# Performance work log

Hardware: AMD Instinct MI355X
Metric: run time of the kernel (lower is better)

Reference implementation:

```python
import jax, jax.numpy as jnp
import numpy as np

NU, NI = 50000, 50000
N = NU + NI
NNZ = 1_000_000
DIM = 64          # dim_latent
FK = 4            # factor_k
DK = DIM // FK    # dim_k = 16
ITER_K = 2        # iterate_k
NUM_LAYER = 2     # len(dim_layer_list)
EPS = 1e-12


def setup_inputs() -> dict:
    key = jax.random.key(0)
    k1, k2, k3, k4 = jax.random.split(key, 4)
    # xavier-ish init scale for the embedding tables
    embed_user = jax.random.normal(k1, (NU, DIM), dtype=jnp.float32) * 0.1
    embed_item = jax.random.normal(k2, (NI, DIM), dtype=jnp.float32) * 0.1
    edge_head = jax.random.randint(k3, (NNZ,), 0, N, dtype=jnp.int32)
    edge_tail = jax.random.randint(k4, (NNZ,), 0, N, dtype=jnp.int32)
    return {"embed_user": embed_user, "embed_item": embed_item,
            "edge_head": edge_head, "edge_tail": edge_tail}


def _l2norm(x, axis=-1):
    # torch F.normalize(p=2): x / max(||x||, eps)
    return x / jnp.maximum(jnp.linalg.norm(x, axis=axis, keepdims=True), EPS)


def _dgcf_forward(embed_user, embed_item, head, tail):
    ego = jnp.concatenate([embed_user, embed_item], axis=0)  # [N, DIM]
    A_values = jnp.ones((FK, NNZ), dtype=ego.dtype)
    all_embed = [ego]

    def spmm(v, x):
        # sparse A (values v on edges head->tail) @ x : [N, DK]
        return jax.ops.segment_sum(v[:, None] * x[tail], head, num_segments=N)

    spmm_f = jax.vmap(spmm)  # over factor axis

    for _ in range(NUM_LAYER):
        # split ego into factor chunks: [FK, N, DK]
        xs = jnp.moveaxis(ego.reshape(N, FK, DK), 1, 0)
        factor_emb = None
        for t in range(ITER_K):
            # softmax over factors per edge; detached (as in torch .detach())
            vals = jax.lax.stop_gradient(jax.nn.softmax(A_values, axis=0))  # [FK, NNZ]
            # row sums of each factor adjacency -> D = diag(1/sqrt(rowsum))
            row_sum = jax.ops.segment_sum(vals.T, head, num_segments=N).T   # [FK, N]
            d = jnp.where(row_sum > 0,
                          1.0 / jnp.sqrt(jnp.maximum(row_sum, EPS)), 0.0)
            # factor_emb = D @ A @ D @ x  (three chained spmm in torch)
            y = spmm_f(vals, d[:, :, None] * xs)
            factor_emb = d[:, :, None] * y                                   # [FK, N, DK]
            # routing scores: sum over dim of normalize(h) * tanh(normalize(t))
            h = _l2norm(factor_emb[:, head, :], -1)                          # [FK, NNZ, DK]
            tt = _l2norm(xs[:, tail, :], -1)
            scores = jnp.sum(h * jnp.tanh(tt), axis=-1)                      # [FK, NNZ]
            A_values = A_values + scores
        # layer output: normalize last-iteration factor embeddings, re-concat
        layer_emb = _l2norm(factor_emb, -1)           # [FK, N, DK]
        ego = jnp.moveaxis(layer_emb, 0, 1).reshape(N, DIM)
        all_embed.append(ego)

    out = jnp.mean(jnp.stack(all_embed, axis=1), axis=1)  # [N, DIM]
    return out


def reference(embed_user, embed_item, edge_head, edge_tail):
    out = _dgcf_forward(embed_user, embed_item, edge_head, edge_tail)
    return out[:NU], out[NU:]
```

## Files before the change

### kernel.cpp

```cpp
#include <hip/hip_runtime.h>
#include <hip/hip_bf16.h>

#define NUSER 50000
#define NITEM 50000
#define NN    100000
#define NNZ_  1000000
#define DIM_  64
#define NBLK  391
#define EPB   2560
#define BINC  4096
#define NPAD  (NBLK * BINC)

#define FL_SVC    1
#define FL_SC     2
#define FL_NEXT   8
#define FL_FIN    16
#define FL_ACONST 32
#define FL_ASTORE 64
#define FL_GN     128

static inline int ceil_div(int a, int b) { return (a + b - 1) / b; }

static __device__ inline float bf2f(unsigned short u) {
    return __uint_as_float(((unsigned int)u) << 16);
}
static __device__ inline unsigned short f2bf(float f) {
    unsigned int x = __float_as_uint(f);
    x += 0x7fffu + ((x >> 16) & 1u);
    return (unsigned short)(x >> 16);
}

#if __has_builtin(__builtin_amdgcn_fdot2_f32_bf16)
typedef __bf16 bf16x2_t __attribute__((ext_vector_type(2)));
static __device__ inline float dot2bf(unsigned int a, unsigned int b, float c) {
    return __builtin_amdgcn_fdot2_f32_bf16(__builtin_bit_cast(bf16x2_t, a),
                                           __builtin_bit_cast(bf16x2_t, b), c, false);
}
#else
static __device__ inline float dot2bf(unsigned int a, unsigned int b, float c) {
    return c + bf2f((unsigned short)(a & 0xffffu)) * bf2f((unsigned short)(b & 0xffffu))
             + bf2f((unsigned short)(a >> 16)) * bf2f((unsigned short)(b >> 16));
}
#endif

__global__ void k_binscat(const int* __restrict__ head, const int* __restrict__ tail,
                          int* __restrict__ cursor, int* __restrict__ bin) {
    __shared__ int cnt[NBLK];
    __shared__ int chunk[NBLK];
    int tid = threadIdx.x;
    for (int i = tid; i < NBLK; i += 256) cnt[i] = 0;
    __syncthreads();
    int e0 = blockIdx.x * EPB;
    int e1 = min(e0 + EPB, NNZ_);
    for (int e = e0 + tid; e < e1; e += 256)
        atomicAdd(&cnt[head[e] >> 8], 1);
    __syncthreads();
    for (int i = tid; i < NBLK; i += 256) {
        chunk[i] = cnt[i] ? (i * BINC + atomicAdd(&cursor[i], cnt[i])) : 0;
        cnt[i] = 0;
    }
    __syncthreads();
    for (int e = e0 + tid; e < e1; e += 256) {
        int h = head[e], t = tail[e];
        int b = h >> 8;
        int off = atomicAdd(&cnt[b], 1);
        bin[chunk[b] + off] = t | ((h & 255) << 20);
    }
}

__global__ void k_bucket(const int* __restrict__ bin, const int* __restrict__ cursor,
                         int2* __restrict__ row_se, float4* __restrict__ d4a,
                         int* __restrict__ csr_tail) {
    __shared__ int deg[256];
    __shared__ int sh[256];
    __shared__ int cur[256];
    int tid = threadIdx.x;
    int b = blockIdx.x;
    int n0 = b << 8;
    int e0 = b * BINC, e1 = e0 + cursor[b];
    deg[tid] = 0;
    __syncthreads();
    for (int e = e0 + tid; e < e1; e += 256)
        atomicAdd(&deg[bin[e] >> 20], 1);
    __syncthreads();
    int myDeg = deg[tid];
    sh[tid] = myDeg;
    __syncthreads();
    for (int off = 1; off < 256; off <<= 1) {
        int u = 0;
        if (tid >= off) u = sh[tid - off];
        __syncthreads();
        sh[tid] += u;
        __syncthreads();
    }
    int loff = sh[tid] - myDeg;
    int start = b * BINC + loff;
    int n = n0 + tid;
    if (n < NN) {
        row_se[n] = make_int2(start, start + myDeg);
        float dd = (myDeg > 0) ? 2.0f / sqrtf((float)myDeg) : 0.0f;
        d4a[n] = make_float4(dd, dd, dd, dd);
    }
    cur[tid] = start;
    __syncthreads();
    for (int e = e0 + tid; e < e1; e += 256) {
        int p = bin[e];
        int pos = atomicAdd(&cur[p >> 20], 1);
        csr_tail[pos] = p & 0xFFFFF;
    }
}

__global__ void k_init(const float* __restrict__ eu, const float* __restrict__ ei,
                       const float* __restrict__ d4a,
                       unsigned short* __restrict__ ego, unsigned short* __restrict__ te,
                       unsigned short* __restrict__ G0, float* __restrict__ out) {
    int i = blockIdx.x * 256 + threadIdx.x;
    if (i >= NN * DIM_) return;
    float v = (i < NUSER * DIM_) ? eu[i] : ei[i - NUSER * DIM_];
    out[i] = v;
    ego[i] = f2bf(v);
    G0[i] = f2bf(v * d4a[i >> 4]);
    float s = v * v;
    s += __shfl_xor(s, 1); s += __shfl_xor(s, 2);
    s += __shfl_xor(s, 4); s += __shfl_xor(s, 8);
    float nrm = v / fmaxf(sqrtf(s), 1e-12f);
    float ex = __expf(2.0f * nrm);
    te[i] = f2bf((ex - 1.0f) / (ex + 1.0f));
}

template<int FLAGS, int NJ>
static __device__ __forceinline__ void iter_body(
    int n, int lane, int q, int l, int f, int r0, int r1,
    unsigned short* __restrict__ svals,
    const unsigned short* __restrict__ G,
    const unsigned short* __restrict__ te,
    const int* __restrict__ csr_tail,
    float* __restrict__ A4,
    float* __restrict__ out,
    const unsigned short* __restrict__ X,
    unsigned short* __restrict__ Gn,
    unsigned short* __restrict__ egon, unsigned short* __restrict__ ten)
{
    float ax = 0.f, ay = 0.f, az = 0.f, aw = 0.f;

    int ct[NJ]; float cw[NJ]; float ca[NJ]; uint2 cv[NJ];
    int eb = r0 + q;
#pragma unroll
    for (int j = 0; j < NJ; ++j) {
        int i = eb + 4 * j;
        bool v = (i < r1);
        int ic = v ? i : r0;
        int t = csr_tail[ic];
        ct[j] = v ? t : 0;
        float w;
        if (FLAGS & FL_SVC) w = 1.0f;
        else w = bf2f(svals[ic * 4 + f]);
        cw[j] = v ? w : 0.f;
        if ((FLAGS & FL_SC) && !(FLAGS & FL_ACONST))
            ca[j] = A4[ic * 4 + f];
    }
#pragma unroll
    for (int j = 0; j < NJ; ++j) {
        if (FLAGS & FL_SC)
            cv[j] = *(const uint2*)(te + ct[j] * 64 + 4 * l);
    }
#pragma unroll
    for (int j = 0; j < NJ; ++j) {
        ushort4 u = *(const ushort4*)(G + ct[j] * 64 + 4 * l);
        ax += cw[j] * bf2f(u.x); ay += cw[j] * bf2f(u.y);
        az += cw[j] * bf2f(u.z); aw += cw[j] * bf2f(u.w);
    }

    if (NJ == 4) {
        for (int base = r0 + 16; base < r1; base += 16) {
            int tj[4]; float wj[4];
#pragma unroll
            for (int j = 0; j < 4; ++j) {
                int i = base + q + 4 * j;
                bool v = (i < r1);
                int ic = v ? i : r0;
                int t = csr_tail[ic];
                tj[j] = v ? t : 0;
                float w;
                if (FLAGS & FL_SVC) w = 1.0f;
                else w = bf2f(svals[ic * 4 + f]);
                wj[j] = v ? w : 0.f;
            }
#pragma unroll
            for (int j = 0; j < 4; ++j) {
                ushort4 u = *(const ushort4*)(G + tj[j] * 64 + 4 * l);
                ax += wj[j] * bf2f(u.x); ay += wj[j] * bf2f(u.y);
                az += wj[j] * bf2f(u.z); aw += wj[j] * bf2f(u.w);
            }
        }
    }

    ax += __shfl_xor(ax, 16); ax += __shfl_xor(ax, 32);
    ay += __shfl_xor(ay, 16); ay += __shfl_xor(ay, 32);
    az += __shfl_xor(az, 16); az += __shfl_xor(az, 32);
    aw += __shfl_xor(aw, 16); aw += __shfl_xor(aw, 32);

    float s = ax * ax + ay * ay + az * az + aw * aw;
    s += __shfl_xor(s, 1); s += __shfl_xor(s, 2);
    float inv = 1.0f / fmaxf(sqrtf(s), 1e-12f);
    float fx = ax * inv, fy = ay * inv, fz = az * inv, fw = aw * inv;

    float y = 0.f;
    if (FLAGS & (FL_NEXT | FL_FIN)) {
        int src = lane >> 2;
        float t0r = __shfl(fx, src), t1r = __shfl(fy, src);
        float t2r = __shfl(fz, src), t3r = __shfl(fw, src);
        y = (lane & 2) ? ((lane & 1) ? t3r : t2r) : ((lane & 1) ? t1r : t0r);
        int base = n * 64 + lane;
        if (FLAGS & FL_FIN) {
            out[base] = (out[base] + bf2f(X[base]) + y) * (1.0f / 3.0f);
        }
        if (FLAGS & FL_NEXT) {
            egon[base] = f2bf(y);
            float e2 = __expf(2.0f * y);
            ten[base] = f2bf((e2 - 1.0f) / (e2 + 1.0f));
        }
    }

    float accs = 0.f;
    if (FLAGS & FL_SC) {
        unsigned int p01 = ((unsigned int)f2bf(fy) << 16) | f2bf(fx);
        unsigned int p23 = ((unsigned int)f2bf(fw) << 16) | f2bf(fz);
#pragma unroll
        for (int j = 0; j < NJ; ++j) {
            int i = eb + 4 * j;
            bool v = (i < r1);
            float dot = dot2bf(cv[j].y, p23, dot2bf(cv[j].x, p01, 0.0f));
            dot += __shfl_xor(dot, 1); dot += __shfl_xor(dot, 2);
            float a = (FLAGS & FL_ACONST) ? 1.0f : ca[j];
            a += dot;
            float ex = __expf(a);
            float sum = ex;
            sum += __shfl_xor(sum, 4); sum += __shfl_xor(sum, 8);
            float sv = ex / sum;
            if (v && (l & 3) == 0) {
                if (FLAGS & FL_ASTORE) A4[i * 4 + f] = a;
                svals[i * 4 + f] = f2bf(sv);
            }
            accs += v ? sv : 0.f;
        }
        if (NJ == 4) {
            for (int base = r0 + 16; base < r1; base += 16) {
                int tj[4]; float aj[4]; uint2 vj[4];
#pragma unroll
                for (int j = 0; j < 4; ++j) {
                    int i = base + q + 4 * j;
                    bool v = (i < r1);
                    int ic = v ? i : r0;
                    int t = csr_tail[ic];
                    tj[j] = v ? t : 0;
                    if (!(FLAGS & FL_ACONST)) aj[j] = A4[ic * 4 + f];
                }
#pragma unroll
                for (int j = 0; j < 4; ++j)
                    vj[j] = *(const uint2*)(te + tj[j] * 64 + 4 * l);
#pragma unroll
                for (int j = 0; j < 4; ++j) {
                    int i = base + q + 4 * j;
                    bool v = (i < r1);
                    float dot = dot2bf(vj[j].y, p23, dot2bf(vj[j].x, p01, 0.0f));
                    dot += __shfl_xor(dot, 1); dot += __shfl_xor(dot, 2);
                    float a = (FLAGS & FL_ACONST) ? 1.0f : aj[j];
                    a += dot;
                    float ex = __expf(a);
                    float sum = ex;
                    sum += __shfl_xor(sum, 4); sum += __shfl_xor(sum, 8);
                    float sv = ex / sum;
                    if (v && (l & 3) == 0) {
                        if (FLAGS & FL_ASTORE) A4[i * 4 + f] = a;
                        svals[i * 4 + f] = f2bf(sv);
                    }
                    accs += v ? sv : 0.f;
                }
            }
        }
        accs += __shfl_xor(accs, 16); accs += __shfl_xor(accs, 32);
    }

    if (FLAGS & (FL_GN | FL_NEXT)) {
        float av = __shfl(accs, (lane >> 4) << 2);
        float d = (av > 0.f) ? 1.0f / sqrtf(fmaxf(av, 1e-12f)) : 0.f;
        int base = n * 64 + lane;
        float src = (FLAGS & FL_NEXT) ? y : bf2f(X[base]);
        Gn[base] = f2bf(src * d);
    }
}

template<int FLAGS>
__global__ void k_iter(unsigned short* __restrict__ svals,
                       const unsigned short* __restrict__ G,
                       const unsigned short* __restrict__ te,
                       const int2* __restrict__ row_se, const int* __restrict__ csr_tail,
                       float* __restrict__ A4,
                       float* __restrict__ out,
                       const unsigned short* __restrict__ X,
                       unsigned short* __restrict__ Gn,
                       unsigned short* __restrict__ egon, unsigned short* __restrict__ ten) {
    int n = (blockIdx.x * 256 + threadIdx.x) >> 6;
    if (n >= NN) return;
    int lane = threadIdx.x & 63;
    int q = lane >> 4;
    int l = lane & 15;
    int f = l >> 2;
    int2 se = row_se[n];
    int r0 = __builtin_amdgcn_readfirstlane(se.x);
    int r1 = __builtin_amdgcn_readfirstlane(se.y);
    int deg = r1 - r0;
    if (deg <= 8) {
        if (deg <= 4)
            iter_body<FLAGS, 1>(n, lane, q, l, f, r0, r1, svals, G, te,
                                csr_tail, A4, out, X, Gn, egon, ten);
        else
            iter_body<FLAGS, 2>(n, lane, q, l, f, r0, r1, svals, G, te,
                                csr_tail, A4, out, X, Gn, egon, ten);
    } else {
        if (deg <= 12)
            iter_body<FLAGS, 3>(n, lane, q, l, f, r0, r1, svals, G, te,
                                csr_tail, A4, out, X, Gn, egon, ten);
        else
            iter_body<FLAGS, 4>(n, lane, q, l, f, r0, r1, svals, G, te,
                                csr_tail, A4, out, X, Gn, egon, ten);
    }
}

extern "C" void kernel_launch(void* const* d_in, const int* in_sizes, int n_in,
                              void* d_out, int out_size, void* d_ws, size_t ws_size,
                              hipStream_t stream) {
    const float* eu = (const float*)d_in[0];
    const float* ei = (const float*)d_in[1];
    const int* head = (const int*)d_in[2];
    const int* tail = (const int*)d_in[3];
    float* out = (float*)d_out;

    float* A4 = (float*)d_ws;
    float* d4a = A4 + (size_t)NPAD * 4;
    unsigned short* svals = (unsigned short*)(d4a + (size_t)NN * 4);
    unsigned short* ego_a = svals + (size_t)NPAD * 4;
    unsigned short* te_a  = ego_a + (size_t)NN * DIM_;
    unsigned short* ego_b = te_a + (size_t)NN * DIM_;
    unsigned short* te_b  = ego_b + (size_t)NN * DIM_;
    unsigned short* Ga    = te_b + (size_t)NN * DIM_;
    unsigned short* Gb    = Ga + (size_t)NN * DIM_;
    int* csr_tail = (int*)(Gb + (size_t)NN * DIM_);
    int2* row_se = (int2*)(csr_tail + (size_t)NPAD);
    int* cursor = (int*)(row_se + NN);
    int* bin = (int*)A4;

    const int node_blocks = ceil_div(NN * DIM_, 256);
    const int wave_blocks = ceil_div(NN * 64, 256);

    hipMemsetAsync(cursor, 0, NBLK * sizeof(int), stream);
    k_binscat<<<NBLK, 256, 0, stream>>>(head, tail, cursor, bin);
    k_bucket<<<NBLK, 256, 0, stream>>>(bin, cursor, row_se, (float4*)d4a, csr_tail);

    k_init<<<node_blocks, 256, 0, stream>>>(eu, ei, d4a, ego_a, te_a, Ga, out);

    k_iter<FL_SVC | FL_SC | FL_ACONST | FL_ASTORE | FL_GN><<<wave_blocks, 256, 0, stream>>>(
        svals, Ga, te_a, row_se, csr_tail, A4, out, ego_a, Gb, ego_b, te_b);

    k_iter<FL_SC | FL_ASTORE | FL_NEXT><<<wave_blocks, 256, 0, stream>>>(
        svals, Gb, te_a, row_se, csr_tail, A4, out, ego_a, Ga, ego_b, te_b);

    k_iter<FL_SC | FL_GN><<<wave_blocks, 256, 0, stream>>>(
        svals, Ga, te_b, row_se, csr_tail, A4, out, ego_b, Gb, ego_b, te_b);

    k_iter<FL_FIN><<<wave_blocks, 256, 0, stream>>>(
        svals, Gb, te_b, row_se, csr_tail, A4, out, ego_b, Ga, ego_b, te_b);
}
```

Measured before the change: 342.1 us.

## Map one node per 16 lanes instead of one node per wavefront

Each node's row is now handled by a 16-lane group, so a wavefront processes four nodes at once rather than one, with each lane walking edges serially. It first unrolls 8 edges, then loops in chunks of 4 up to the wavefront's maximum degree. The cross-quarter shuffle reductions go away, and outputs are written as vectorized ushort4/float4 per lane. This aims to remove the idle lanes that low-degree rows (about 10 edges on average) left in a full wavefront, at the cost of divergence when the four rows in a wavefront have different degrees, plus higher register use from the 8-wide unroll.

```diff
diff --git a/kernel.cpp b/kernel.cpp
--- a/kernel.cpp
+++ b/kernel.cpp
@@ -128,169 +128,6 @@
     te[i] = f2bf((ex - 1.0f) / (ex + 1.0f));
 }
 
-template<int FLAGS, int NJ>
-static __device__ __forceinline__ void iter_body(
-    int n, int lane, int q, int l, int f, int r0, int r1,
-    unsigned short* __restrict__ svals,
-    const unsigned short* __restrict__ G,
-    const unsigned short* __restrict__ te,
-    const int* __restrict__ csr_tail,
-    float* __restrict__ A4,
-    float* __restrict__ out,
-    const unsigned short* __restrict__ X,
-    unsigned short* __restrict__ Gn,
-    unsigned short* __restrict__ egon, unsigned short* __restrict__ ten)
-{
-    float ax = 0.f, ay = 0.f, az = 0.f, aw = 0.f;
-
-    int ct[NJ]; float cw[NJ]; float ca[NJ]; uint2 cv[NJ];
-    int eb = r0 + q;
-#pragma unroll
-    for (int j = 0; j < NJ; ++j) {
-        int i = eb + 4 * j;
-        bool v = (i < r1);
-        int ic = v ? i : r0;
-        int t = csr_tail[ic];
-        ct[j] = v ? t : 0;
-        float w;
-        if (FLAGS & FL_SVC) w = 1.0f;
-        else w = bf2f(svals[ic * 4 + f]);
-        cw[j] = v ? w : 0.f;
-        if ((FLAGS & FL_SC) && !(FLAGS & FL_ACONST))
-            ca[j] = A4[ic * 4 + f];
-    }
-#pragma unroll
-    for (int j = 0; j < NJ; ++j) {
-        if (FLAGS & FL_SC)
-            cv[j] = *(const uint2*)(te + ct[j] * 64 + 4 * l);
-    }
-#pragma unroll
-    for (int j = 0; j < NJ; ++j) {
-        ushort4 u = *(const ushort4*)(G + ct[j] * 64 + 4 * l);
-        ax += cw[j] * bf2f(u.x); ay += cw[j] * bf2f(u.y);
-        az += cw[j] * bf2f(u.z); aw += cw[j] * bf2f(u.w);
-    }
-
-    if (NJ == 4) {
-        for (int base = r0 + 16; base < r1; base += 16) {
-            int tj[4]; float wj[4];
-#pragma unroll
-            for (int j = 0; j < 4; ++j) {
-                int i = base + q + 4 * j;
-                bool v = (i < r1);
-                int ic = v ? i : r0;
-                int t = csr_tail[ic];
-                tj[j] = v ? t : 0;
-                float w;
-                if (FLAGS & FL_SVC) w = 1.0f;
-                else w = bf2f(svals[ic * 4 + f]);
-                wj[j] = v ? w : 0.f;
-            }
-#pragma unroll
-            for (int j = 0; j < 4; ++j) {
-                ushort4 u = *(const ushort4*)(G + tj[j] * 64 + 4 * l);
-                ax += wj[j] * bf2f(u.x); ay += wj[j] * bf2f(u.y);
-                az += wj[j] * bf2f(u.z); aw += wj[j] * bf2f(u.w);
-            }
-        }
-    }
-
-    ax += __shfl_xor(ax, 16); ax += __shfl_xor(ax, 32);
-    ay += __shfl_xor(ay, 16); ay += __shfl_xor(ay, 32);
-    az += __shfl_xor(az, 16); az += __shfl_xor(az, 32);
-    aw += __shfl_xor(aw, 16); aw += __shfl_xor(aw, 32);
-
-    float s = ax * ax + ay * ay + az * az + aw * aw;
-    s += __shfl_xor(s, 1); s += __shfl_xor(s, 2);
-    float inv = 1.0f / fmaxf(sqrtf(s), 1e-12f);
-    float fx = ax * inv, fy = ay * inv, fz = az * inv, fw = aw * inv;
-
-    float y = 0.f;
-    if (FLAGS & (FL_NEXT | FL_FIN)) {
-        int src = lane >> 2;
-        float t0r = __shfl(fx, src), t1r = __shfl(fy, src);
-        float t2r = __shfl(fz, src), t3r = __shfl(fw, src);
-        y = (lane & 2) ? ((lane & 1) ? t3r : t2r) : ((lane & 1) ? t1r : t0r);
-        int base = n * 64 + lane;
-        if (FLAGS & FL_FIN) {
-            out[base] = (out[base] + bf2f(X[base]) + y) * (1.0f / 3.0f);
-        }
-        if (FLAGS & FL_NEXT) {
-            egon[base] = f2bf(y);
-            float e2 = __expf(2.0f * y);
-            ten[base] = f2bf((e2 - 1.0f) / (e2 + 1.0f));
-        }
-    }
-
-    float accs = 0.f;
-    if (FLAGS & FL_SC) {
-        unsigned int p01 = ((unsigned int)f2bf(fy) << 16) | f2bf(fx);
-        unsigned int p23 = ((unsigned int)f2bf(fw) << 16) | f2bf(fz);
-#pragma unroll
-        for (int j = 0; j < NJ; ++j) {
-            int i = eb + 4 * j;
-            bool v = (i < r1);
-            float dot = dot2bf(cv[j].y, p23, dot2bf(cv[j].x, p01, 0.0f));
-            dot += __shfl_xor(dot, 1); dot += __shfl_xor(dot, 2);
-            float a = (FLAGS & FL_ACONST) ? 1.0f : ca[j];
-            a += dot;
-            float ex = __expf(a);
-            float sum = ex;
-            sum += __shfl_xor(sum, 4); sum += __shfl_xor(sum, 8);
-            float sv = ex / sum;
-            if (v && (l & 3) == 0) {
-                if (FLAGS & FL_ASTORE) A4[i * 4 + f] = a;
-                svals[i * 4 + f] = f2bf(sv);
-            }
-            accs += v ? sv : 0.f;
-        }
-        if (NJ == 4) {
-            for (int base = r0 + 16; base < r1; base += 16) {
-                int tj[4]; float aj[4]; uint2 vj[4];
-#pragma unroll
-                for (int j = 0; j < 4; ++j) {
-                    int i = base + q + 4 * j;
-                    bool v = (i < r1);
-                    int ic = v ? i : r0;
-                    int t = csr_tail[ic];
-                    tj[j] = v ? t : 0;
-                    if (!(FLAGS & FL_ACONST)) aj[j] = A4[ic * 4 + f];
-                }
-#pragma unroll
-                for (int j = 0; j < 4; ++j)
-                    vj[j] = *(const uint2*)(te + tj[j] * 64 + 4 * l);
-#pragma unroll
-                for (int j = 0; j < 4; ++j) {
-                    int i = base + q + 4 * j;
-                    bool v = (i < r1);
-                    float dot = dot2bf(vj[j].y, p23, dot2bf(vj[j].x, p01, 0.0f));
-                    dot += __shfl_xor(dot, 1); dot += __shfl_xor(dot, 2);
-                    float a = (FLAGS & FL_ACONST) ? 1.0f : aj[j];
-                    a += dot;
-                    float ex = __expf(a);
-                    float sum = ex;
-                    sum += __shfl_xor(sum, 4); sum += __shfl_xor(sum, 8);
-                    float sv = ex / sum;
-                    if (v && (l & 3) == 0) {
-                        if (FLAGS & FL_ASTORE) A4[i * 4 + f] = a;
-                        svals[i * 4 + f] = f2bf(sv);
-                    }
-                    accs += v ? sv : 0.f;
-                }
-            }
-        }
-        accs += __shfl_xor(accs, 16); accs += __shfl_xor(accs, 32);
-    }
-
-    if (FLAGS & (FL_GN | FL_NEXT)) {
-        float av = __shfl(accs, (lane >> 4) << 2);
-        float d = (av > 0.f) ? 1.0f / sqrtf(fmaxf(av, 1e-12f)) : 0.f;
-        int base = n * 64 + lane;
-        float src = (FLAGS & FL_NEXT) ? y : bf2f(X[base]);
-        Gn[base] = f2bf(src * d);
-    }
-}
-
 template<int FLAGS>
 __global__ void k_iter(unsigned short* __restrict__ svals,
                        const unsigned short* __restrict__ G,
@@ -300,31 +137,168 @@
                        float* __restrict__ out,
                        const unsigned short* __restrict__ X,
                        unsigned short* __restrict__ Gn,
-                       unsigned short* __restrict__ egon, unsigned short* __restrict__ ten) {
-    int n = (blockIdx.x * 256 + threadIdx.x) >> 6;
+                       unsigned short* __restrict__ egon, unsigned short* __restrict__ ten)
+{
+    int n = (blockIdx.x * 256 + threadIdx.x) >> 4;
     if (n >= NN) return;
-    int lane = threadIdx.x & 63;
-    int q = lane >> 4;
-    int l = lane & 15;
-    int f = l >> 2;
+    int l16 = threadIdx.x & 15;
+    int f = l16 >> 2;
     int2 se = row_se[n];
-    int r0 = __builtin_amdgcn_readfirstlane(se.x);
-    int r1 = __builtin_amdgcn_readfirstlane(se.y);
-    int deg = r1 - r0;
-    if (deg <= 8) {
-        if (deg <= 4)
-            iter_body<FLAGS, 1>(n, lane, q, l, f, r0, r1, svals, G, te,
-                                csr_tail, A4, out, X, Gn, egon, ten);
-        else
-            iter_body<FLAGS, 2>(n, lane, q, l, f, r0, r1, svals, G, te,
-                                csr_tail, A4, out, X, Gn, egon, ten);
-    } else {
-        if (deg <= 12)
-            iter_body<FLAGS, 3>(n, lane, q, l, f, r0, r1, svals, G, te,
-                                csr_tail, A4, out, X, Gn, egon, ten);
-        else
-            iter_body<FLAGS, 4>(n, lane, q, l, f, r0, r1, svals, G, te,
-                                csr_tail, A4, out, X, Gn, egon, ten);
+    int r0 = se.x;
+    int deg = se.y - se.x;
+    int m = deg;
+    m = max(m, __shfl_xor(m, 16));
+    m = max(m, __shfl_xor(m, 32));
+    int maxdeg = __builtin_amdgcn_readfirstlane(m);
+
+    float ax = 0.f, ay = 0.f, az = 0.f, aw = 0.f;
+
+    int ct[8]; float cw[8]; float ca[8]; uint2 cv[8];
+#pragma unroll
+    for (int j = 0; j < 8; ++j) {
+        bool v = (j < deg);
+        int ic = v ? (r0 + j) : r0;
+        int t = csr_tail[ic];
+        ct[j] = v ? t : 0;
+        float w;
+        if (FLAGS & FL_SVC) w = 1.0f;
+        else w = bf2f(svals[ic * 4 + f]);
+        cw[j] = v ? w : 0.f;
+        if ((FLAGS & FL_SC) && !(FLAGS & FL_ACONST))
+            ca[j] = A4[ic * 4 + f];
+    }
+#pragma unroll
+    for (int j = 0; j < 8; ++j) {
+        if (FLAGS & FL_SC)
+            cv[j] = *(const uint2*)(te + ct[j] * 64 + 4 * l16);
+    }
+#pragma unroll
+    for (int j = 0; j < 8; ++j) {
+        ushort4 u = *(const ushort4*)(G + ct[j] * 64 + 4 * l16);
+        ax += cw[j] * bf2f(u.x); ay += cw[j] * bf2f(u.y);
+        az += cw[j] * bf2f(u.z); aw += cw[j] * bf2f(u.w);
+    }
+
+    for (int kb = 8; kb < maxdeg; kb += 4) {
+        int tj[4]; float wj[4];
+#pragma unroll
+        for (int j = 0; j < 4; ++j) {
+            int jj = kb + j;
+            bool v = (jj < deg);
+            int ic = v ? (r0 + jj) : r0;
+            int t = csr_tail[ic];
+            tj[j] = v ? t : 0;
+            float w;
+            if (FLAGS & FL_SVC) w = 1.0f;
+            else w = bf2f(svals[ic * 4 + f]);
+            wj[j] = v ? w : 0.f;
+        }
+#pragma unroll
+        for (int j = 0; j < 4; ++j) {
+            ushort4 u = *(const ushort4*)(G + tj[j] * 64 + 4 * l16);
+            ax += wj[j] * bf2f(u.x); ay += wj[j] * bf2f(u.y);
+            az += wj[j] * bf2f(u.z); aw += wj[j] * bf2f(u.w);
+        }
+    }
+
+    float s = ax * ax + ay * ay + az * az + aw * aw;
+    s += __shfl_xor(s, 1); s += __shfl_xor(s, 2);
+    float inv = 1.0f / fmaxf(sqrtf(s), 1e-12f);
+    float fx = ax * inv, fy = ay * inv, fz = az * inv, fw = aw * inv;
+
+    int base = n * 64 + 4 * l16;
+    if (FLAGS & FL_FIN) {
+        float4* po = (float4*)(out + base);
+        float4 ov = *po;
+        ushort4 xv = *(const ushort4*)(X + base);
+        ov.x = (ov.x + bf2f(xv.x) + fx) * (1.0f / 3.0f);
+        ov.y = (ov.y + bf2f(xv.y) + fy) * (1.0f / 3.0f);
+        ov.z = (ov.z + bf2f(xv.z) + fz) * (1.0f / 3.0f);
+        ov.w = (ov.w + bf2f(xv.w) + fw) * (1.0f / 3.0f);
+        *po = ov;
+    }
+    if (FLAGS & FL_NEXT) {
+        ushort4 o;
+        o.x = f2bf(fx); o.y = f2bf(fy); o.z = f2bf(fz); o.w = f2bf(fw);
+        *(ushort4*)(egon + base) = o;
+        float e0 = __expf(2.0f * fx), e1 = __expf(2.0f * fy);
+        float e2 = __expf(2.0f * fz), e3 = __expf(2.0f * fw);
+        ushort4 p;
+        p.x = f2bf((e0 - 1.0f) / (e0 + 1.0f)); p.y = f2bf((e1 - 1.0f) / (e1 + 1.0f));
+        p.z = f2bf((e2 - 1.0f) / (e2 + 1.0f)); p.w = f2bf((e3 - 1.0f) / (e3 + 1.0f));
+        *(ushort4*)(ten + base) = p;
+    }
+
+    float accs = 0.f;
+    if (FLAGS & FL_SC) {
+        unsigned int p01 = ((unsigned int)f2bf(fy) << 16) | f2bf(fx);
+        unsigned int p23 = ((unsigned int)f2bf(fw) << 16) | f2bf(fz);
+#pragma unroll
+        for (int j = 0; j < 8; ++j) {
+            bool v = (j < deg);
+            int i = r0 + j;
+            float dot = dot2bf(cv[j].y, p23, dot2bf(cv[j].x, p01, 0.0f));
+            dot += __shfl_xor(dot, 1); dot += __shfl_xor(dot, 2);
+            float a = (FLAGS & FL_ACONST) ? 1.0f : ca[j];
+            a += dot;
+            float ex = __expf(a);
+            float sum = ex;
+            sum += __shfl_xor(sum, 4); sum += __shfl_xor(sum, 8);
+            float sv = ex / sum;
+            if (v && (l16 & 3) == 0) {
+                if (FLAGS & FL_ASTORE) A4[i * 4 + f] = a;
+                svals[i * 4 + f] = f2bf(sv);
+            }
+            accs += v ? sv : 0.f;
+        }
+        for (int kb = 8; kb < maxdeg; kb += 4) {
+            int tj[4]; float aj[4]; uint2 vj[4];
+#pragma unroll
+            for (int j = 0; j < 4; ++j) {
+                int jj = kb + j;
+                bool v = (jj < deg);
+                int ic = v ? (r0 + jj) : r0;
+                int t = csr_tail[ic];
+                tj[j] = v ? t : 0;
+                if (!(FLAGS & FL_ACONST)) aj[j] = A4[ic * 4 + f];
+            }
+#pragma unroll
+            for (int j = 0; j < 4; ++j)
+                vj[j] = *(const uint2*)(te + tj[j] * 64 + 4 * l16);
+#pragma unroll
+            for (int j = 0; j < 4; ++j) {
+                int jj = kb + j;
+                bool v = (jj < deg);
+                int i = r0 + jj;
+                float dot = dot2bf(vj[j].y, p23, dot2bf(vj[j].x, p01, 0.0f));
+                dot += __shfl_xor(dot, 1); dot += __shfl_xor(dot, 2);
+                float a = (FLAGS & FL_ACONST) ? 1.0f : aj[j];
+                a += dot;
+                float ex = __expf(a);
+                float sum = ex;
+                sum += __shfl_xor(sum, 4); sum += __shfl_xor(sum, 8);
+                float sv = ex / sum;
+                if (v && (l16 & 3) == 0) {
+                    if (FLAGS & FL_ASTORE) A4[i * 4 + f] = a;
+                    svals[i * 4 + f] = f2bf(sv);
+                }
+                accs += v ? sv : 0.f;
+            }
+        }
+    }
+
+    if (FLAGS & (FL_GN | FL_NEXT)) {
+        float d = (accs > 0.f) ? 1.0f / sqrtf(fmaxf(accs, 1e-12f)) : 0.f;
+        float sx, sy, sz, sw;
+        if (FLAGS & FL_NEXT) { sx = fx; sy = fy; sz = fz; sw = fw; }
+        else {
+            ushort4 xv = *(const ushort4*)(X + base);
+            sx = bf2f(xv.x); sy = bf2f(xv.y); sz = bf2f(xv.z); sw = bf2f(xv.w);
+        }
+        ushort4 o;
+        o.x = f2bf(sx * d); o.y = f2bf(sy * d);
+        o.z = f2bf(sz * d); o.w = f2bf(sw * d);
+        *(ushort4*)(Gn + base) = o;
     }
 }
 
@@ -352,7 +326,7 @@
     int* bin = (int*)A4;
 
     const int node_blocks = ceil_div(NN * DIM_, 256);
-    const int wave_blocks = ceil_div(NN * 64, 256);
+    const int iter_blocks = ceil_div(NN * 16, 256);
 
     hipMemsetAsync(cursor, 0, NBLK * sizeof(int), stream);
     k_binscat<<<NBLK, 256, 0, stream>>>(head, tail, cursor, bin);
@@ -360,15 +334,15 @@
 
     k_init<<<node_blocks, 256, 0, stream>>>(eu, ei, d4a, ego_a, te_a, Ga, out);
 
-    k_iter<FL_SVC | FL_SC | FL_ACONST | FL_ASTORE | FL_GN><<<wave_blocks, 256, 0, stream>>>(
+    k_iter<FL_SVC | FL_SC | FL_ACONST | FL_ASTORE | FL_GN><<<iter_blocks, 256, 0, stream>>>(
         svals, Ga, te_a, row_se, csr_tail, A4, out, ego_a, Gb, ego_b, te_b);
 
-    k_iter<FL_SC | FL_ASTORE | FL_NEXT><<<wave_blocks, 256, 0, stream>>>(
+    k_iter<FL_SC | FL_ASTORE | FL_NEXT><<<iter_blocks, 256, 0, stream>>>(
         svals, Gb, te_a, row_se, csr_tail, A4, out, ego_a, Ga, ego_b, te_b);
 
-    k_iter<FL_SC | FL_GN><<<wave_blocks, 256, 0, stream>>>(
+    k_iter<FL_SC | FL_GN><<<iter_blocks, 256, 0, stream>>>(
         svals, Ga, te_b, row_se, csr_tail, A4, out, ego_b, Gb, ego_b, te_b);
 
-    k_iter<FL_FIN><<<wave_blocks, 256, 0, stream>>>(
+    k_iter<FL_FIN><<<iter_blocks, 256, 0, stream>>>(
         svals, Gb, te_b, row_se, csr_tail, A4, out, ego_b, Ga, ego_b, te_b);
 }
```

Result: no change. 341.4 us (-0.2%).
